# Kernel optimization log

Measured on AMD Instinct MI355X. Metric: run time of the kernel, lower is better.

Reference implementation:

```python
import jax, jax.numpy as jnp
import numpy as np

N_ENT = 100000
N_USR = 1024
E = 400000
D = 128
H = 4
R = 32


def setup_inputs() -> dict:
    key = jax.random.key(0)
    ks = jax.random.split(key, 9)
    a = float(np.sqrt(6.0 / (D + D)))  # xavier_uniform bound for [D, D]
    return {
        "entity_emb": jax.random.normal(ks[0], (N_ENT, D), dtype=jnp.float32),
        "user_emb": jax.random.normal(ks[1], (N_USR, D), dtype=jnp.float32),
        "interact_mat": jnp.zeros((1,), dtype=jnp.float32),  # unused by forward
        "weight": jax.random.normal(ks[2], (R, D), dtype=jnp.float32) * 0.1,
        "qTrans": jax.random.uniform(ks[3], (D, D), minval=-a, maxval=a, dtype=jnp.float32),
        "kTrans": jax.random.uniform(ks[4], (D, D), minval=-a, maxval=a, dtype=jnp.float32),
        "vTrans": jax.random.uniform(ks[5], (D, D), minval=-a, maxval=a, dtype=jnp.float32),
        "edge_index": jax.random.randint(ks[6], (2, E), 0, N_ENT, dtype=jnp.int64)
            if jax.config.jax_enable_x64 else jax.random.randint(ks[6], (2, E), 0, N_ENT, dtype=jnp.int32),
        "edge_type": jax.random.randint(ks[7], (E,), 1, R + 1, dtype=jnp.int32),  # types in [1, R]
        "layer": 0,
    }


def _kglayer(rows, col_embeds, embeds, n_seg, qT, kT, vT):
    # rows: [E] target-node index, col_embeds: [E, D] edge messages
    dh = D // H
    row_embeds = embeds[rows]                              # gather [E, D]
    q = (row_embeds @ qT).reshape(-1, H, dh)
    k = (col_embeds @ kT).reshape(-1, H, dh)
    v = (col_embeds @ vT).reshape(-1, H, dh)
    att = jnp.clip(jnp.einsum("ehd,ehd->eh", q, k), -10.0, 10.0)
    exp_att = jnp.exp(att)                                 # [E, H]
    att_norm = jax.ops.segment_sum(exp_att, rows, num_segments=n_seg)[rows]
    att = exp_att / (att_norm + 1e-8)
    res = (att[..., None] * v).reshape(-1, D)              # [E, D]
    return jax.ops.segment_sum(res, rows, num_segments=n_seg)


def _sim_hrt(head_emb, tail_emb, rel_emb):
    # per-edge scalar attention logit [E, 1]
    tr = jnp.linalg.norm(tail_emb * rel_emb, axis=1, keepdims=True)
    hr = jnp.linalg.norm(head_emb * rel_emb, axis=1, keepdims=True)
    return (hr * tr) ** 2


def reference(entity_emb, user_emb, interact_mat, weight, qTrans, kTrans, vTrans,
              edge_index, edge_type, layer):
    n_entities = entity_emb.shape[0]
    head, tail = edge_index[0], edge_index[1]
    rel = weight[edge_type - 1]                            # [E, D]
    neigh = entity_emb[tail] * rel                         # [E, D]
    kg_emb = _kglayer(head, neigh, entity_emb, n_entities, qTrans, kTrans, vTrans)
    w = _sim_hrt(kg_emb[head], kg_emb[tail], rel)          # [E, 1]
    w = jnp.broadcast_to(w, neigh.shape)                   # expand to [E, D]
    # scatter_softmax over edges sharing the same head (numerically stable)
    m = jax.ops.segment_max(w, head, num_segments=n_entities)[head]
    e = jnp.exp(w - m)
    s = jax.ops.segment_sum(e, head, num_segments=n_entities)[head]
    soft = e / s
    msg = soft * entity_emb[tail]
    return jax.ops.segment_sum(msg, head, num_segments=n_entities)
```

## Files before the change

### kernel.cpp

```cpp
#include <hip/hip_runtime.h>
#include <cstdint>

#define D 128
#define H 4
#define N_ENT 100000
#define N_EDGE 400000
#define R 32

#define SCAN_NB ((N_ENT + 511) / 512)

__global__ void k_hist(const int* __restrict__ head, int* __restrict__ deg) {
  const int e = blockIdx.x * 256 + threadIdx.x;
  if (e < N_EDGE) atomicAdd(&deg[head[e]], 1);
}

__global__ __launch_bounds__(256) void k_scan1(const int* __restrict__ deg,
                                               int* __restrict__ bsum) {
  const int t = threadIdx.x;
  const int i = blockIdx.x * 512 + t * 2;
  int v0 = (i < N_ENT) ? deg[i] : 0;
  int v1 = (i + 1 < N_ENT) ? deg[i + 1] : 0;
  int s = v0 + v1;
#pragma unroll
  for (int k = 1; k < 64; k <<= 1) s += __shfl_xor(s, k);
  __shared__ int ws[4];
  if ((t & 63) == 0) ws[t >> 6] = s;
  __syncthreads();
  if (t == 0) bsum[blockIdx.x] = ws[0] + ws[1] + ws[2] + ws[3];
}

__global__ __launch_bounds__(256) void k_scan2(const int* __restrict__ bsum,
                                               int* __restrict__ bbase,
                                               int* __restrict__ off) {
  __shared__ int sh[256];
  const int t = threadIdx.x;
  const int v = (t < SCAN_NB) ? bsum[t] : 0;
  sh[t] = v;
  __syncthreads();
  for (int d = 1; d < 256; d <<= 1) {
    const int u = (t >= d) ? sh[t - d] : 0;
    __syncthreads();
    sh[t] += u;
    __syncthreads();
  }
  if (t < SCAN_NB) bbase[t] = sh[t] - v;
  if (t == SCAN_NB - 1) off[N_ENT] = sh[t];
}

__global__ __launch_bounds__(256) void k_scan3(const int* __restrict__ deg,
                                               const int* __restrict__ bbase,
                                               int* __restrict__ off,
                                               int* __restrict__ cur) {
  __shared__ int sh[256];
  const int t = threadIdx.x;
  const int i = blockIdx.x * 512 + t * 2;
  const int v0 = (i < N_ENT) ? deg[i] : 0;
  const int v1 = (i + 1 < N_ENT) ? deg[i + 1] : 0;
  const int s = v0 + v1;
  sh[t] = s;
  __syncthreads();
  for (int d = 1; d < 256; d <<= 1) {
    const int u = (t >= d) ? sh[t - d] : 0;
    __syncthreads();
    sh[t] += u;
    __syncthreads();
  }
  const int ex = sh[t] - s + bbase[blockIdx.x];
  if (i < N_ENT) {
    off[i] = ex;
    cur[i] = ex;
  }
  if (i + 1 < N_ENT) {
    off[i + 1] = ex + v0;
    cur[i + 1] = ex + v0;
  }
}

__global__ void k_scatter(const int* __restrict__ head,
                          const int* __restrict__ tail,
                          const int* __restrict__ etype, int* __restrict__ cur,
                          int2* __restrict__ teP) {
  const int e = blockIdx.x * 256 + threadIdx.x;
  if (e >= N_EDGE) return;
  const int hd = head[e];
  const int pos = atomicAdd(&cur[hd], 1);
  teP[pos] = make_int2(tail[e], etype[e] - 1);
}

__global__ __launch_bounds__(256) void k_tr(const float* __restrict__ in,
                                            float* __restrict__ out) {
  __shared__ float tile[32][33];
  const int bx = blockIdx.x & 3, by = blockIdx.x >> 2;
  const int c = threadIdx.x & 31;
  const int r0 = (threadIdx.x >> 5) * 4;
#pragma unroll
  for (int i = 0; i < 4; ++i)
    tile[r0 + i][c] = in[(by * 32 + r0 + i) * 128 + bx * 32 + c];
  __syncthreads();
#pragma unroll
  for (int i = 0; i < 4; ++i)
    out[(bx * 32 + r0 + i) * 128 + by * 32 + c] = tile[c][r0 + i];
}

__global__ __launch_bounds__(512) void k_qproj(const float* __restrict__ ent,
                                               const float* __restrict__ qT,
                                               float* __restrict__ Q) {
  __shared__ float sT[D * D];
  __shared__ float rows[D * 128];
  const int t = threadIdx.x;
  const int n0 = blockIdx.x * 128;
#pragma unroll
  for (int s = 0; s < 8; ++s) {
    const int idx = (s * 512 + t) * 4;
    *(float4*)&sT[idx] = *(const float4*)&qT[idx];
  }
  {
    const int g = t & 3;
    const int n = t >> 2;
    const int node = n0 + n;
    if (node < N_ENT) {
      const float* src = ent + (size_t)node * D;
#pragma unroll
      for (int s = 0; s < 8; ++s) {
        const int i = s * 16 + g * 4;
        float4 v = *(const float4*)&src[i];
        rows[(i + 0) * 128 + n] = v.x;
        rows[(i + 1) * 128 + n] = v.y;
        rows[(i + 2) * 128 + n] = v.z;
        rows[(i + 3) * 128 + n] = v.w;
      }
    } else {
#pragma unroll
      for (int s = 0; s < 8; ++s) {
        const int i = s * 16 + g * 4;
        rows[(i + 0) * 128 + n] = 0.f;
        rows[(i + 1) * 128 + n] = 0.f;
        rows[(i + 2) * 128 + n] = 0.f;
        rows[(i + 3) * 128 + n] = 0.f;
      }
    }
  }
  __syncthreads();
  const int jj = t & 15;
  const int ee = t >> 4;
  float acc[4][8];
#pragma unroll
  for (int a = 0; a < 4; ++a)
#pragma unroll
    for (int b = 0; b < 8; ++b) acc[a][b] = 0.f;
#pragma unroll 4
  for (int i = 0; i < D; ++i) {
    float4 b0 = *(float4*)&sT[i * D + jj * 8];
    float4 b1 = *(float4*)&sT[i * D + jj * 8 + 4];
    float4 a0 = *(float4*)&rows[i * 128 + ee * 4];
    float bv[8] = {b0.x, b0.y, b0.z, b0.w, b1.x, b1.y, b1.z, b1.w};
    float av[4] = {a0.x, a0.y, a0.z, a0.w};
#pragma unroll
    for (int a = 0; a < 4; ++a)
#pragma unroll
      for (int b = 0; b < 8; ++b) acc[a][b] = fmaf(av[a], bv[b], acc[a][b]);
  }
#pragma unroll
  for (int a = 0; a < 4; ++a) {
    const int node = n0 + ee * 4 + a;
    if (node < N_ENT) {
      float4 o0 = {acc[a][0], acc[a][1], acc[a][2], acc[a][3]};
      float4 o1 = {acc[a][4], acc[a][5], acc[a][6], acc[a][7]};
      *(float4*)&Q[(size_t)node * D + jj * 8] = o0;
      *(float4*)&Q[(size_t)node * D + jj * 8 + 4] = o1;
    }
  }
}

__global__ __launch_bounds__(256, 4) void k_fused(
    const float* __restrict__ ent, const float* __restrict__ wrel,
    const float* __restrict__ kTt, const float* __restrict__ vT, float* qkg,
    const int* __restrict__ off, const int2* __restrict__ teP) {
  __shared__ float sQ[8 * 128];
  __shared__ float sP[8 * 512];
  __shared__ float sAgg[8 * 512];
  const int t = threadIdx.x;
  const int base = blockIdx.x * 8;

  {
    const int k = t >> 5;
    const int c4 = (t & 31) * 4;
    *(float4*)&sQ[k * 128 + c4] =
        *(const float4*)&qkg[(size_t)(base + k) * D + c4];
  }
  __syncthreads();

  {
    const int i = t & 127;
    const int sub = t >> 7;
    float pp[2][8];
#pragma unroll
    for (int hh = 0; hh < 2; ++hh)
#pragma unroll
      for (int k = 0; k < 8; ++k) pp[hh][k] = 0.f;
#pragma unroll
    for (int hh = 0; hh < 2; ++hh) {
      const int h = sub * 2 + hh;
#pragma unroll 8
      for (int c = 0; c < 32; ++c) {
        const float kv = kTt[(h * 32 + c) * 128 + i];
#pragma unroll
        for (int k = 0; k < 8; ++k)
          pp[hh][k] = fmaf(kv, sQ[k * 128 + h * 32 + c], pp[hh][k]);
      }
    }
#pragma unroll
    for (int hh = 0; hh < 2; ++hh)
#pragma unroll
      for (int k = 0; k < 8; ++k)
        sP[k * 512 + (sub * 2 + hh) * 128 + i] = pp[hh][k];
  }
  __syncthreads();

  {
    const int wid = t >> 6;
    const int half = (t >> 5) & 1;
    const int l32 = t & 31;
    const int k = wid * 2 + half;
    const int n = base + k;
    const int lp = l32 & 3;
    const float4 P0 = *(const float4*)&sP[k * 512 + 0 * 128 + l32 * 4];
    const float4 P1 = *(const float4*)&sP[k * 512 + 1 * 128 + l32 * 4];
    const float4 P2 = *(const float4*)&sP[k * 512 + 2 * 128 + l32 * 4];
    const float4 P3 = *(const float4*)&sP[k * 512 + 3 * 128 + l32 * 4];
    float4 b0 = {0, 0, 0, 0}, b1 = {0, 0, 0, 0};
    float4 b2 = {0, 0, 0, 0}, b3 = {0, 0, 0, 0};
    float s0 = 0.f, s1 = 0.f, s2 = 0.f, s3 = 0.f;
    const int eb = off[n];
    const int deg = off[n + 1] - eb;
    float4 xv = {0, 0, 0, 0}, rv = {0, 0, 0, 0};
    if (deg > 0) {
      const int2 pf = teP[eb];
      xv = *(const float4*)&ent[(size_t)pf.x * D + l32 * 4];
      rv = *(const float4*)&wrel[(size_t)pf.y * D + l32 * 4];
    }
    for (int idx = 0; idx < deg; ++idx) {
      const float4 cx = xv, cr = rv;
      if (idx + 1 < deg) {
        const int2 pf = teP[eb + idx + 1];
        xv = *(const float4*)&ent[(size_t)pf.x * D + l32 * 4];
        rv = *(const float4*)&wrel[(size_t)pf.y * D + l32 * 4];
      }
      const float4 nh = {cx.x * cr.x, cx.y * cr.y, cx.z * cr.z, cx.w * cr.w};
      float d0 = nh.x * P0.x + nh.y * P0.y + nh.z * P0.z + nh.w * P0.w;
      float d1 = nh.x * P1.x + nh.y * P1.y + nh.z * P1.z + nh.w * P1.w;
      float d2 = nh.x * P2.x + nh.y * P2.y + nh.z * P2.z + nh.w * P2.w;
      float d3 = nh.x * P3.x + nh.y * P3.y + nh.z * P3.z + nh.w * P3.w;
      float x01 = (l32 & 1) ? d1 : d0;
      float y01 = (l32 & 1) ? d0 : d1;
      x01 += __shfl_xor(y01, 1);
      float x23 = (l32 & 1) ? d3 : d2;
      float y23 = (l32 & 1) ? d2 : d3;
      x23 += __shfl_xor(y23, 1);
      float xa = (l32 & 2) ? x23 : x01;
      float xb = (l32 & 2) ? x01 : x23;
      xa += __shfl_xor(xb, 2);
      xa += __shfl_xor(xa, 4);
      xa += __shfl_xor(xa, 8);
      xa += __shfl_xor(xa, 16);
      const float eL = expf(fminf(fmaxf(xa, -10.f), 10.f));
      const float e0 = eL;
      const float e1 = __shfl_xor(eL, 1);
      const float e2 = __shfl_xor(eL, 2);
      const float e3 = __shfl_xor(eL, 3);
      b0.x = fmaf(e0, nh.x, b0.x); b0.y = fmaf(e0, nh.y, b0.y);
      b0.z = fmaf(e0, nh.z, b0.z); b0.w = fmaf(e0, nh.w, b0.w);
      b1.x = fmaf(e1, nh.x, b1.x); b1.y = fmaf(e1, nh.y, b1.y);
      b1.z = fmaf(e1, nh.z, b1.z); b1.w = fmaf(e1, nh.w, b1.w);
      b2.x = fmaf(e2, nh.x, b2.x); b2.y = fmaf(e2, nh.y, b2.y);
      b2.z = fmaf(e2, nh.z, b2.z); b2.w = fmaf(e2, nh.w, b2.w);
      b3.x = fmaf(e3, nh.x, b3.x); b3.y = fmaf(e3, nh.y, b3.y);
      b3.z = fmaf(e3, nh.z, b3.z); b3.w = fmaf(e3, nh.w, b3.w);
      s0 += e0; s1 += e1; s2 += e2; s3 += e3;
    }
    const float i0 = 1.f / (s0 + 1e-8f);
    const float i1 = 1.f / (s1 + 1e-8f);
    const float i2 = 1.f / (s2 + 1e-8f);
    const float i3 = 1.f / (s3 + 1e-8f);
    float4 o0 = {b0.x * i0, b0.y * i0, b0.z * i0, b0.w * i0};
    float4 o1 = {b1.x * i1, b1.y * i1, b1.z * i1, b1.w * i1};
    float4 o2 = {b2.x * i2, b2.y * i2, b2.z * i2, b2.w * i2};
    float4 o3 = {b3.x * i3, b3.y * i3, b3.z * i3, b3.w * i3};
    const int sb = k * 512 + l32 * 4;
    *(float4*)&sAgg[sb + ((lp ^ 0) << 7)] = o0;
    *(float4*)&sAgg[sb + ((lp ^ 1) << 7)] = o1;
    *(float4*)&sAgg[sb + ((lp ^ 2) << 7)] = o2;
    *(float4*)&sAgg[sb + ((lp ^ 3) << 7)] = o3;
  }
  __syncthreads();

  {
    const int c = t & 127;
    const int g4 = (t >> 7) * 4;
    const int h = c >> 5;
    float acc0 = 0.f, acc1 = 0.f, acc2 = 0.f, acc3 = 0.f;
    const float* agg0 = &sAgg[(g4 + 0) * 512 + h * 128];
    const float* agg1 = &sAgg[(g4 + 1) * 512 + h * 128];
    const float* agg2 = &sAgg[(g4 + 2) * 512 + h * 128];
    const float* agg3 = &sAgg[(g4 + 3) * 512 + h * 128];
#pragma unroll 4
    for (int d = 0; d < 128; ++d) {
      const float v = vT[d * 128 + c];
      acc0 = fmaf(agg0[d], v, acc0);
      acc1 = fmaf(agg1[d], v, acc1);
      acc2 = fmaf(agg2[d], v, acc2);
      acc3 = fmaf(agg3[d], v, acc3);
    }
    qkg[(size_t)(base + g4 + 0) * D + c] = acc0;
    qkg[(size_t)(base + g4 + 1) * D + c] = acc1;
    qkg[(size_t)(base + g4 + 2) * D + c] = acc2;
    qkg[(size_t)(base + g4 + 3) * D + c] = acc3;
  }
}

__global__ __launch_bounds__(256) void k_S(const float* __restrict__ kg,
                                           const float* __restrict__ wrel,
                                           float* __restrict__ S) {
  __shared__ float sB[D * 32];
  __shared__ float sA[D * 64];
  const int t = threadIdx.x;
  const int n0 = blockIdx.x * 64;
  {
    const int r = t & 31;
    const int qg = t >> 5;
#pragma unroll
    for (int s = 0; s < 4; ++s) {
      const int d = qg * 16 + s * 4;
      float4 b = *(const float4*)&wrel[(size_t)r * D + d];
      sB[(d + 0) * 32 + r] = b.x * b.x;
      sB[(d + 1) * 32 + r] = b.y * b.y;
      sB[(d + 2) * 32 + r] = b.z * b.z;
      sB[(d + 3) * 32 + r] = b.w * b.w;
    }
  }
  {
    const int nn = t & 63;
    const int dg = t >> 6;
    const int node = n0 + nn;
#pragma unroll
    for (int s = 0; s < 8; ++s) {
      const int d = dg * 32 + s * 4;
      float4 a = {0, 0, 0, 0};
      if (node < N_ENT) a = *(const float4*)&kg[(size_t)node * D + d];
      sA[(d + 0) * 64 + nn] = a.x * a.x;
      sA[(d + 1) * 64 + nn] = a.y * a.y;
      sA[(d + 2) * 64 + nn] = a.z * a.z;
      sA[(d + 3) * 64 + nn] = a.w * a.w;
    }
  }
  __syncthreads();
  const int nn2 = t >> 2;
  const int rg = t & 3;
  float acc[8];
#pragma unroll
  for (int c = 0; c < 8; ++c) acc[c] = 0.f;
#pragma unroll 4
  for (int d = 0; d < D; ++d) {
    const float a = sA[d * 64 + nn2];
    float4 b0 = *(float4*)&sB[d * 32 + rg * 8];
    float4 b1 = *(float4*)&sB[d * 32 + rg * 8 + 4];
    acc[0] = fmaf(a, b0.x, acc[0]);
    acc[1] = fmaf(a, b0.y, acc[1]);
    acc[2] = fmaf(a, b0.z, acc[2]);
    acc[3] = fmaf(a, b0.w, acc[3]);
    acc[4] = fmaf(a, b1.x, acc[4]);
    acc[5] = fmaf(a, b1.y, acc[5]);
    acc[6] = fmaf(a, b1.z, acc[6]);
    acc[7] = fmaf(a, b1.w, acc[7]);
  }
  const int node = n0 + nn2;
  if (node < N_ENT) {
    float4 o0 = {acc[0], acc[1], acc[2], acc[3]};
    float4 o1 = {acc[4], acc[5], acc[6], acc[7]};
    *(float4*)&S[(size_t)node * 32 + rg * 8] = o0;
    *(float4*)&S[(size_t)node * 32 + rg * 8 + 4] = o1;
  }
}

__global__ __launch_bounds__(256) void k_out2(
    const float* __restrict__ ent, const float* __restrict__ S,
    const int* __restrict__ off, const int2* __restrict__ teP,
    float* __restrict__ out) {
  const int t = threadIdx.x;
  const int wid = t >> 6;
  const int lane = t & 63;
  const int n = blockIdx.x * 4 + wid;
  if (n >= N_ENT) return;
  const int eb = off[n];
  const int deg = off[n + 1] - eb;
  float accx = 0.f, accy = 0.f;
  float m = 0.f, ssum = 0.f;
  for (int b = 0; b < deg; b += 64) {
    const int idx = b + lane;
    const bool val = idx < deg;
    const int e = eb + (val ? idx : 0);
    const int2 tp = teP[e];
    const int tl = tp.x;
    const int ty = tp.y;
    float w = val ? S[(size_t)n * 32 + ty] * S[(size_t)tl * 32 + ty] : -1.f;
    float cm = w;
#pragma unroll
    for (int k = 1; k < 64; k <<= 1) cm = fmaxf(cm, __shfl_xor(cm, k));
    const float mnew = fmaxf(m, cm);
    const float scale = expf(m - mnew);
    const float el = val ? expf(w - mnew) : 0.f;
    float cs = el;
#pragma unroll
    for (int k = 1; k < 64; k <<= 1) cs += __shfl_xor(cs, k);
    ssum = ssum * scale + cs;
    accx *= scale;
    accy *= scale;
    const int cnt = (deg - b < 64) ? deg - b : 64;
    {
      const int tl0 = __shfl(tl, 0);
      float2 xr = *(const float2*)&ent[(size_t)tl0 * D + lane * 2];
      for (int j = 0; j < cnt; ++j) {
        const float sj = __shfl(el, j);
        const float2 cx = xr;
        if (j + 1 < cnt) {
          const int tlj = __shfl(tl, j + 1);
          xr = *(const float2*)&ent[(size_t)tlj * D + lane * 2];
        }
        accx = fmaf(sj, cx.x, accx);
        accy = fmaf(sj, cx.y, accy);
      }
    }
    m = mnew;
  }
  const float inv = (deg > 0) ? 1.f / ssum : 0.f;
  float2 o = {accx * inv, accy * inv};
  *(float2*)&out[(size_t)n * D + lane * 2] = o;
}

extern "C" void kernel_launch(void* const* d_in, const int* in_sizes, int n_in,
                              void* d_out, int out_size, void* d_ws,
                              size_t ws_size, hipStream_t stream) {
  const float* ent = (const float*)d_in[0];
  const float* wrel = (const float*)d_in[3];
  const float* qT = (const float*)d_in[4];
  const float* kT = (const float*)d_in[5];
  const float* vT = (const float*)d_in[6];
  const int* eidx = (const int*)d_in[7];
  const int* etype = (const int*)d_in[8];
  const int* head = eidx;
  const int* tail = eidx + N_EDGE;

  float* S = (float*)d_ws;
  int* off = (int*)(S + (size_t)N_ENT * 32);
  int* cur = off + (N_ENT + 2);
  int* deg = cur + N_ENT;
  int* bsum = deg + N_ENT;
  int* bbase = bsum + SCAN_NB;
  int2* teP = (int2*)(bbase + SCAN_NB);
  float* kTt = (float*)(teP + N_EDGE);
  float* qkg = (float*)d_out;

  hipMemsetAsync(deg, 0, N_ENT * sizeof(int), stream);
  k_hist<<<(N_EDGE + 255) / 256, 256, 0, stream>>>(head, deg);
  k_scan1<<<SCAN_NB, 256, 0, stream>>>(deg, bsum);
  k_scan2<<<1, 256, 0, stream>>>(bsum, bbase, off);
  k_scan3<<<SCAN_NB, 256, 0, stream>>>(deg, bbase, off, cur);
  k_scatter<<<(N_EDGE + 255) / 256, 256, 0, stream>>>(head, tail, etype, cur,
                                                      teP);
  k_tr<<<16, 256, 0, stream>>>(kT, kTt);
  k_qproj<<<(N_ENT + 127) / 128, 512, 0, stream>>>(ent, qT, qkg);
  k_fused<<<N_ENT / 8, 256, 0, stream>>>(ent, wrel, kTt, vT, qkg, off, teP);
  k_S<<<(N_ENT + 63) / 64, 256, 0, stream>>>(qkg, wrel, S);
  k_out2<<<(N_ENT + 3) / 4, 256, 0, stream>>>(ent, S, off, teP, qkg);
}
```

Baseline: 522.0 us.

## Merge shared buffers, raise occupancy, hoist edge prefetch, vectorize LDS reads, fast exp

The sP and sAgg shared arrays are merged into one buffer, cutting LDS per block so that launch bounds can target 8 blocks per CU instead of 4. The first edge gather and the offset loads are moved ahead of the first barrier so their latency overlaps the Q load and the P matmul. The P and V matmul loops now read shared memory as float4 to issue fewer LDS instructions, and expf is replaced by __expf in two kernels. The tighter launch bound may cause register spills, and __expf is slightly less accurate.

```diff
diff --git a/kernel.cpp b/kernel.cpp
--- a/kernel.cpp
+++ b/kernel.cpp
@@ -172,15 +172,20 @@
   }
 }
 
-__global__ __launch_bounds__(256, 4) void k_fused(
+__global__ __launch_bounds__(256, 8) void k_fused(
     const float* __restrict__ ent, const float* __restrict__ wrel,
     const float* __restrict__ kTt, const float* __restrict__ vT, float* qkg,
     const int* __restrict__ off, const int2* __restrict__ teP) {
   __shared__ float sQ[8 * 128];
-  __shared__ float sP[8 * 512];
-  __shared__ float sAgg[8 * 512];
+  __shared__ float sPA[8 * 512];
   const int t = threadIdx.x;
   const int base = blockIdx.x * 8;
+
+  const int wid = t >> 6;
+  const int half = (t >> 5) & 1;
+  const int l32 = t & 31;
+  const int kk = wid * 2 + half;
+  const int n = base + kk;
 
   {
     const int k = t >> 5;
@@ -188,6 +193,15 @@
     *(float4*)&sQ[k * 128 + c4] =
         *(const float4*)&qkg[(size_t)(base + k) * D + c4];
   }
+
+  const int eb = off[n];
+  const int deg = off[n + 1] - eb;
+  float4 xv = {0, 0, 0, 0}, rv = {0, 0, 0, 0};
+  if (deg > 0) {
+    const int2 pf = teP[eb];
+    xv = *(const float4*)&ent[(size_t)pf.x * D + l32 * 4];
+    rv = *(const float4*)&wrel[(size_t)pf.y * D + l32 * 4];
+  }
   __syncthreads();
 
   {
@@ -201,44 +215,39 @@
 #pragma unroll
     for (int hh = 0; hh < 2; ++hh) {
       const int h = sub * 2 + hh;
-#pragma unroll 8
-      for (int c = 0; c < 32; ++c) {
-        const float kv = kTt[(h * 32 + c) * 128 + i];
-#pragma unroll
-        for (int k = 0; k < 8; ++k)
-          pp[hh][k] = fmaf(kv, sQ[k * 128 + h * 32 + c], pp[hh][k]);
+#pragma unroll 2
+      for (int c4 = 0; c4 < 8; ++c4) {
+        const float kv0 = kTt[(h * 32 + c4 * 4 + 0) * 128 + i];
+        const float kv1 = kTt[(h * 32 + c4 * 4 + 1) * 128 + i];
+        const float kv2 = kTt[(h * 32 + c4 * 4 + 2) * 128 + i];
+        const float kv3 = kTt[(h * 32 + c4 * 4 + 3) * 128 + i];
+#pragma unroll
+        for (int k = 0; k < 8; ++k) {
+          const float4 q = *(const float4*)&sQ[k * 128 + h * 32 + c4 * 4];
+          pp[hh][k] = fmaf(kv0, q.x, pp[hh][k]);
+          pp[hh][k] = fmaf(kv1, q.y, pp[hh][k]);
+          pp[hh][k] = fmaf(kv2, q.z, pp[hh][k]);
+          pp[hh][k] = fmaf(kv3, q.w, pp[hh][k]);
+        }
       }
     }
 #pragma unroll
     for (int hh = 0; hh < 2; ++hh)
 #pragma unroll
       for (int k = 0; k < 8; ++k)
-        sP[k * 512 + (sub * 2 + hh) * 128 + i] = pp[hh][k];
-  }
-  __syncthreads();
-
-  {
-    const int wid = t >> 6;
-    const int half = (t >> 5) & 1;
-    const int l32 = t & 31;
-    const int k = wid * 2 + half;
-    const int n = base + k;
+        sPA[k * 512 + (sub * 2 + hh) * 128 + i] = pp[hh][k];
+  }
+  __syncthreads();
+
+  {
     const int lp = l32 & 3;
-    const float4 P0 = *(const float4*)&sP[k * 512 + 0 * 128 + l32 * 4];
-    const float4 P1 = *(const float4*)&sP[k * 512 + 1 * 128 + l32 * 4];
-    const float4 P2 = *(const float4*)&sP[k * 512 + 2 * 128 + l32 * 4];
-    const float4 P3 = *(const float4*)&sP[k * 512 + 3 * 128 + l32 * 4];
+    const float4 P0 = *(const float4*)&sPA[kk * 512 + 0 * 128 + l32 * 4];
+    const float4 P1 = *(const float4*)&sPA[kk * 512 + 1 * 128 + l32 * 4];
+    const float4 P2 = *(const float4*)&sPA[kk * 512 + 2 * 128 + l32 * 4];
+    const float4 P3 = *(const float4*)&sPA[kk * 512 + 3 * 128 + l32 * 4];
     float4 b0 = {0, 0, 0, 0}, b1 = {0, 0, 0, 0};
     float4 b2 = {0, 0, 0, 0}, b3 = {0, 0, 0, 0};
     float s0 = 0.f, s1 = 0.f, s2 = 0.f, s3 = 0.f;
-    const int eb = off[n];
-    const int deg = off[n + 1] - eb;
-    float4 xv = {0, 0, 0, 0}, rv = {0, 0, 0, 0};
-    if (deg > 0) {
-      const int2 pf = teP[eb];
-      xv = *(const float4*)&ent[(size_t)pf.x * D + l32 * 4];
-      rv = *(const float4*)&wrel[(size_t)pf.y * D + l32 * 4];
-    }
     for (int idx = 0; idx < deg; ++idx) {
       const float4 cx = xv, cr = rv;
       if (idx + 1 < deg) {
@@ -263,7 +272,7 @@
       xa += __shfl_xor(xa, 4);
       xa += __shfl_xor(xa, 8);
       xa += __shfl_xor(xa, 16);
-      const float eL = expf(fminf(fmaxf(xa, -10.f), 10.f));
+      const float eL = __expf(fminf(fmaxf(xa, -10.f), 10.f));
       const float e0 = eL;
       const float e1 = __shfl_xor(eL, 1);
       const float e2 = __shfl_xor(eL, 2);
@@ -286,11 +295,11 @@
     float4 o1 = {b1.x * i1, b1.y * i1, b1.z * i1, b1.w * i1};
     float4 o2 = {b2.x * i2, b2.y * i2, b2.z * i2, b2.w * i2};
     float4 o3 = {b3.x * i3, b3.y * i3, b3.z * i3, b3.w * i3};
-    const int sb = k * 512 + l32 * 4;
-    *(float4*)&sAgg[sb + ((lp ^ 0) << 7)] = o0;
-    *(float4*)&sAgg[sb + ((lp ^ 1) << 7)] = o1;
-    *(float4*)&sAgg[sb + ((lp ^ 2) << 7)] = o2;
-    *(float4*)&sAgg[sb + ((lp ^ 3) << 7)] = o3;
+    const int sb = kk * 512 + l32 * 4;
+    *(float4*)&sPA[sb + ((lp ^ 0) << 7)] = o0;
+    *(float4*)&sPA[sb + ((lp ^ 1) << 7)] = o1;
+    *(float4*)&sPA[sb + ((lp ^ 2) << 7)] = o2;
+    *(float4*)&sPA[sb + ((lp ^ 3) << 7)] = o3;
   }
   __syncthreads();
 
@@ -299,17 +308,28 @@
     const int g4 = (t >> 7) * 4;
     const int h = c >> 5;
     float acc0 = 0.f, acc1 = 0.f, acc2 = 0.f, acc3 = 0.f;
-    const float* agg0 = &sAgg[(g4 + 0) * 512 + h * 128];
-    const float* agg1 = &sAgg[(g4 + 1) * 512 + h * 128];
-    const float* agg2 = &sAgg[(g4 + 2) * 512 + h * 128];
-    const float* agg3 = &sAgg[(g4 + 3) * 512 + h * 128];
+    const float* agg0 = &sPA[(g4 + 0) * 512 + h * 128];
+    const float* agg1 = &sPA[(g4 + 1) * 512 + h * 128];
+    const float* agg2 = &sPA[(g4 + 2) * 512 + h * 128];
+    const float* agg3 = &sPA[(g4 + 3) * 512 + h * 128];
 #pragma unroll 4
-    for (int d = 0; d < 128; ++d) {
-      const float v = vT[d * 128 + c];
-      acc0 = fmaf(agg0[d], v, acc0);
-      acc1 = fmaf(agg1[d], v, acc1);
-      acc2 = fmaf(agg2[d], v, acc2);
-      acc3 = fmaf(agg3[d], v, acc3);
+    for (int d4 = 0; d4 < 32; ++d4) {
+      const float4 a0 = *(const float4*)&agg0[d4 * 4];
+      const float4 a1 = *(const float4*)&agg1[d4 * 4];
+      const float4 a2 = *(const float4*)&agg2[d4 * 4];
+      const float4 a3 = *(const float4*)&agg3[d4 * 4];
+      const float v0 = vT[(d4 * 4 + 0) * 128 + c];
+      const float v1 = vT[(d4 * 4 + 1) * 128 + c];
+      const float v2 = vT[(d4 * 4 + 2) * 128 + c];
+      const float v3 = vT[(d4 * 4 + 3) * 128 + c];
+      acc0 = fmaf(a0.x, v0, acc0); acc0 = fmaf(a0.y, v1, acc0);
+      acc0 = fmaf(a0.z, v2, acc0); acc0 = fmaf(a0.w, v3, acc0);
+      acc1 = fmaf(a1.x, v0, acc1); acc1 = fmaf(a1.y, v1, acc1);
+      acc1 = fmaf(a1.z, v2, acc1); acc1 = fmaf(a1.w, v3, acc1);
+      acc2 = fmaf(a2.x, v0, acc2); acc2 = fmaf(a2.y, v1, acc2);
+      acc2 = fmaf(a2.z, v2, acc2); acc2 = fmaf(a2.w, v3, acc2);
+      acc3 = fmaf(a3.x, v0, acc3); acc3 = fmaf(a3.y, v1, acc3);
+      acc3 = fmaf(a3.z, v2, acc3); acc3 = fmaf(a3.w, v3, acc3);
     }
     qkg[(size_t)(base + g4 + 0) * D + c] = acc0;
     qkg[(size_t)(base + g4 + 1) * D + c] = acc1;
@@ -407,8 +427,8 @@
 #pragma unroll
     for (int k = 1; k < 64; k <<= 1) cm = fmaxf(cm, __shfl_xor(cm, k));
     const float mnew = fmaxf(m, cm);
-    const float scale = expf(m - mnew);
-    const float el = val ? expf(w - mnew) : 0.f;
+    const float scale = __expf(m - mnew);
+    const float el = val ? __expf(w - mnew) : 0.f;
     float cs = el;
 #pragma unroll
     for (int k = 1; k < 64; k <<= 1) cs += __shfl_xor(cs, k);
```

Result: no change. 512.1 us (-1.9%).
